# Kernel tuning notes

Hardware: AMD Instinct MI355X
Metric: run time of the kernel (lower is better)

The kernel has to match this reference:

```python
import jax, jax.numpy as jnp
import numpy as np

VOCAB = 50000
COVOCAB = 50000
D = 300
NUM_SENSES = 4
B = 100000


def _xavier(key, shape):
    fan_in, fan_out = shape[-2], shape[-1]
    if len(shape) == 3:
        fan_in, fan_out = shape[1], shape[2]
    limit = (6.0 / (fan_in + fan_out)) ** 0.5
    return jax.random.uniform(key, shape, jnp.float32, -limit, limit)


def setup_inputs() -> dict:
    key = jax.random.key(0)
    k1, k2, k3, k4, k5 = jax.random.split(key, 5)
    V = _xavier(k1, (VOCAB, D, NUM_SENSES))
    W = _xavier(k2, (COVOCAB, D, NUM_SENSES))
    vb = _xavier(k3, (VOCAB, NUM_SENSES))
    wb = _xavier(k4, (COVOCAB, NUM_SENSES))
    IJ = jax.random.randint(k5, (B, 2), 0, VOCAB, dtype=jnp.int64)
    return {"V": V, "W": W, "vb": vb, "wb": wb, "IJ": IJ}


def reference(V, W, vb, wb, IJ):
    i = IJ[:, 0]
    j = IJ[:, 1]
    Vg = V[i]            # [B, d, s_v]  gather
    Wg = W[j]            # [B, d, s_w]  gather
    # bmm(W[j]^T, V[i]) -> [B, s_w, s_v]
    mat = jnp.einsum("bds,bdt->bst", Wg, Vg)
    bias = wb[j][:, :, None] + vb[i][:, None, :]   # [B, s_w, s_v]
    mat = mat + bias
    # faithful to original: log(sum(exp(.)))
    return jnp.log(jnp.sum(jnp.exp(mat), axis=(1, 2)))
```

## Files before the change

### kernel.cpp

```cpp
#include <hip/hip_runtime.h>
#include <hip/hip_bf16.h>


constexpr int D  = 300;
constexpr int NS = 4;

typedef unsigned short ushort8 __attribute__((ext_vector_type(8)));

__device__ __forceinline__ float b2f(unsigned short u) {
    return __uint_as_float(((unsigned int)u) << 16);
}

__global__ void detect_kernel(const unsigned int* __restrict__ Vw,
                              const unsigned int* __restrict__ IJw,
                              int* __restrict__ flags)
{
    const int lane = threadIdx.x & 63;
    unsigned int w0 = Vw[2 * lane];
    unsigned int w1 = Vw[2 * lane + 1];
    unsigned int e0 = (w0 >> 7) & 0xFFu;
    unsigned int e1 = (w1 >> 7) & 0xFFu;
    bool big = (e0 >= 126u) || (e1 >= 126u);
    bool odd_nonzero = (lane < 32) ? (IJw[2 * lane + 1] != 0u) : false;
    int isF32 = __any(big) ? 1 : 0;
    int isI64 = __any(odd_nonzero) ? 0 : 1;
    if (threadIdx.x == 0) {
        flags[0] = isF32;
        flags[1] = isI64;
    }
}

__global__ __launch_bounds__(256) void multisense_kernel(
    const void* __restrict__ V_,
    const void* __restrict__ W_,
    const void* __restrict__ vb_,
    const void* __restrict__ wb_,
    const int*  __restrict__ IJ32,
    void*       __restrict__ out_,
    int B,
    const int*  __restrict__ flags)
{
    const int lane = threadIdx.x & 63;
    const int b    = blockIdx.x * (blockDim.x >> 6) + (threadIdx.x >> 6);
    if (b >= B) return;

    const int isF32 = flags[0];
    const int isI64 = flags[1];

    int i, j;
    if (isI64) { i = IJ32[4 * b]; j = IJ32[4 * b + 2]; }
    else       { i = IJ32[2 * b]; j = IJ32[2 * b + 1]; }

    float acc[NS][NS];
#pragma unroll
    for (int s = 0; s < NS; ++s)
#pragma unroll
        for (int t = 0; t < NS; ++t)
            acc[s][t] = 0.0f;

    if (isF32) {
        const float* Vr = (const float*)V_ + (size_t)i * (D * NS);
        const float* Wr = (const float*)W_ + (size_t)j * (D * NS);
#pragma unroll
        for (int k = 0; k < 5; ++k) {
            const int d = lane + 64 * k;
            if (d < D) {
                const float4 v4 = *reinterpret_cast<const float4*>(Vr + d * NS);
                const float4 w4 = *reinterpret_cast<const float4*>(Wr + d * NS);
                const float v[NS] = {v4.x, v4.y, v4.z, v4.w};
                const float w[NS] = {w4.x, w4.y, w4.z, w4.w};
#pragma unroll
                for (int s = 0; s < NS; ++s)
#pragma unroll
                    for (int t = 0; t < NS; ++t)
                        acc[s][t] = fmaf(w[s], v[t], acc[s][t]);
            }
        }
    } else {
        const unsigned short* Vr = (const unsigned short*)V_ + (size_t)i * (D * NS);
        const unsigned short* Wr = (const unsigned short*)W_ + (size_t)j * (D * NS);
#pragma unroll
        for (int k = 0; k < 3; ++k) {
            const int d = 2 * lane + 128 * k;
            if (d < D) {
                const ushort8 v8 = *reinterpret_cast<const ushort8*>(Vr + d * NS);
                const ushort8 w8 = *reinterpret_cast<const ushort8*>(Wr + d * NS);
                float v[8], w[8];
#pragma unroll
                for (int e = 0; e < 8; ++e) {
                    v[e] = b2f(v8[e]);
                    w[e] = b2f(w8[e]);
                }
#pragma unroll
                for (int s = 0; s < NS; ++s)
#pragma unroll
                    for (int t = 0; t < NS; ++t) {
                        acc[s][t] = fmaf(w[s],     v[t],     acc[s][t]);
                        acc[s][t] = fmaf(w[4 + s], v[4 + t], acc[s][t]);
                    }
            }
        }
    }

#pragma unroll
    for (int off = 32; off; off >>= 1)
#pragma unroll
        for (int s = 0; s < NS; ++s)
#pragma unroll
            for (int t = 0; t < NS; ++t)
                acc[s][t] += __shfl_xor(acc[s][t], off, 64);

    if (lane == 0) {
        float wbj[NS], vbi[NS];
        if (isF32) {
            const float* vbp = (const float*)vb_;
            const float* wbp = (const float*)wb_;
#pragma unroll
            for (int s = 0; s < NS; ++s) {
                wbj[s] = wbp[(size_t)j * NS + s];
                vbi[s] = vbp[(size_t)i * NS + s];
            }
        } else {
            const unsigned short* vbp = (const unsigned short*)vb_;
            const unsigned short* wbp = (const unsigned short*)wb_;
#pragma unroll
            for (int s = 0; s < NS; ++s) {
                wbj[s] = b2f(wbp[(size_t)j * NS + s]);
                vbi[s] = b2f(vbp[(size_t)i * NS + s]);
            }
        }
        float sum = 0.0f;
#pragma unroll
        for (int s = 0; s < NS; ++s)
#pragma unroll
            for (int t = 0; t < NS; ++t)
                sum += expf(acc[s][t] + wbj[s] + vbi[t]);
        const float res = logf(sum);
        if (isF32) ((float*)out_)[b] = res;
        else       ((__hip_bfloat16*)out_)[b] = __float2bfloat16(res);
    }
}

extern "C" void kernel_launch(void* const* d_in, const int* in_sizes, int n_in,
                              void* d_out, int out_size, void* d_ws, size_t ws_size,
                              hipStream_t stream) {
    const void* V  = d_in[0];
    const void* W  = d_in[1];
    const void* vb = d_in[2];
    const void* wb = d_in[3];
    const int*  IJ = (const int*)d_in[4];
    int* flags = (int*)d_ws;

    const int B = out_size;
    hipLaunchKernelGGL(detect_kernel, dim3(1), dim3(64), 0, stream,
                       (const unsigned int*)V, (const unsigned int*)IJ, flags);

    const int wavesPerBlock = 4;
    dim3 block(256);
    dim3 grid((B + wavesPerBlock - 1) / wavesPerBlock);
    hipLaunchKernelGGL(multisense_kernel, grid, block, 0, stream,
                       V, W, vb, wb, IJ, d_out, B, flags);
}
```

Baseline: 510.4 us.

## Drop dtype-detect launch, use butterfly transpose-reduce and parallel exp across lanes

```diff
diff --git a/kernel.cpp b/kernel.cpp
--- a/kernel.cpp
+++ b/kernel.cpp
@@ -2,162 +2,129 @@
 #include <hip/hip_bf16.h>
 
 
-constexpr int D  = 300;
-constexpr int NS = 4;
-
-typedef unsigned short ushort8 __attribute__((ext_vector_type(8)));
-
-__device__ __forceinline__ float b2f(unsigned short u) {
-    return __uint_as_float(((unsigned int)u) << 16);
-}
-
-__global__ void detect_kernel(const unsigned int* __restrict__ Vw,
-                              const unsigned int* __restrict__ IJw,
-                              int* __restrict__ flags)
-{
-    const int lane = threadIdx.x & 63;
-    unsigned int w0 = Vw[2 * lane];
-    unsigned int w1 = Vw[2 * lane + 1];
-    unsigned int e0 = (w0 >> 7) & 0xFFu;
-    unsigned int e1 = (w1 >> 7) & 0xFFu;
-    bool big = (e0 >= 126u) || (e1 >= 126u);
-    bool odd_nonzero = (lane < 32) ? (IJw[2 * lane + 1] != 0u) : false;
-    int isF32 = __any(big) ? 1 : 0;
-    int isI64 = __any(odd_nonzero) ? 0 : 1;
-    if (threadIdx.x == 0) {
-        flags[0] = isF32;
-        flags[1] = isI64;
-    }
-}
+constexpr int D   = 300;
+constexpr int NS  = 4;
+constexpr int ROW = D * NS;
 
 __global__ __launch_bounds__(256) void multisense_kernel(
-    const void* __restrict__ V_,
-    const void* __restrict__ W_,
-    const void* __restrict__ vb_,
-    const void* __restrict__ wb_,
-    const int*  __restrict__ IJ32,
-    void*       __restrict__ out_,
-    int B,
-    const int*  __restrict__ flags)
+    const float* __restrict__ V,
+    const float* __restrict__ W,
+    const float* __restrict__ vb,
+    const float* __restrict__ wb,
+    const unsigned int* __restrict__ IJw,
+    float* __restrict__ out,
+    int B)
 {
     const int lane = threadIdx.x & 63;
     const int b    = blockIdx.x * (blockDim.x >> 6) + (threadIdx.x >> 6);
     if (b >= B) return;
 
-    const int isF32 = flags[0];
-    const int isI64 = flags[1];
+    unsigned int probe = (lane < 32) ? IJw[2 * lane + 1] : 0u;
+    const bool isI64 = (__ballot(probe != 0u) == 0ull);
 
     int i, j;
-    if (isI64) { i = IJ32[4 * b]; j = IJ32[4 * b + 2]; }
-    else       { i = IJ32[2 * b]; j = IJ32[2 * b + 1]; }
+    if (isI64) { i = (int)IJw[4 * (size_t)b];     j = (int)IJw[4 * (size_t)b + 2]; }
+    else       { i = (int)IJw[2 * (size_t)b];     j = (int)IJw[2 * (size_t)b + 1]; }
 
-    float acc[NS][NS];
+    const float* __restrict__ Vr = V + (size_t)i * ROW;
+    const float* __restrict__ Wr = W + (size_t)j * ROW;
+
+    const int s_idx = (lane >> 4) & 3;
+    const int t_idx = (lane >> 2) & 3;
+
+    const float wbj = wb[(size_t)j * NS + s_idx];
+    const float vbi = vb[(size_t)i * NS + t_idx];
+
+    float4 va[5], wa[5];
 #pragma unroll
-    for (int s = 0; s < NS; ++s)
-#pragma unroll
-        for (int t = 0; t < NS; ++t)
-            acc[s][t] = 0.0f;
-
-    if (isF32) {
-        const float* Vr = (const float*)V_ + (size_t)i * (D * NS);
-        const float* Wr = (const float*)W_ + (size_t)j * (D * NS);
-#pragma unroll
-        for (int k = 0; k < 5; ++k) {
-            const int d = lane + 64 * k;
-            if (d < D) {
-                const float4 v4 = *reinterpret_cast<const float4*>(Vr + d * NS);
-                const float4 w4 = *reinterpret_cast<const float4*>(Wr + d * NS);
-                const float v[NS] = {v4.x, v4.y, v4.z, v4.w};
-                const float w[NS] = {w4.x, w4.y, w4.z, w4.w};
-#pragma unroll
-                for (int s = 0; s < NS; ++s)
-#pragma unroll
-                    for (int t = 0; t < NS; ++t)
-                        acc[s][t] = fmaf(w[s], v[t], acc[s][t]);
-            }
-        }
-    } else {
-        const unsigned short* Vr = (const unsigned short*)V_ + (size_t)i * (D * NS);
-        const unsigned short* Wr = (const unsigned short*)W_ + (size_t)j * (D * NS);
-#pragma unroll
-        for (int k = 0; k < 3; ++k) {
-            const int d = 2 * lane + 128 * k;
-            if (d < D) {
-                const ushort8 v8 = *reinterpret_cast<const ushort8*>(Vr + d * NS);
-                const ushort8 w8 = *reinterpret_cast<const ushort8*>(Wr + d * NS);
-                float v[8], w[8];
-#pragma unroll
-                for (int e = 0; e < 8; ++e) {
-                    v[e] = b2f(v8[e]);
-                    w[e] = b2f(w8[e]);
-                }
-#pragma unroll
-                for (int s = 0; s < NS; ++s)
-#pragma unroll
-                    for (int t = 0; t < NS; ++t) {
-                        acc[s][t] = fmaf(w[s],     v[t],     acc[s][t]);
-                        acc[s][t] = fmaf(w[4 + s], v[4 + t], acc[s][t]);
-                    }
-            }
-        }
+    for (int k = 0; k < 4; ++k) {
+        const int d = lane + 64 * k;
+        va[k] = *reinterpret_cast<const float4*>(Vr + (size_t)d * NS);
+        wa[k] = *reinterpret_cast<const float4*>(Wr + (size_t)d * NS);
+    }
+    {
+        const int  d4 = 256 + lane;
+        const int  dc = (d4 < D) ? d4 : 0;
+        const float m = (d4 < D) ? 1.0f : 0.0f;
+        va[4] = *reinterpret_cast<const float4*>(Vr + (size_t)dc * NS);
+        wa[4] = *reinterpret_cast<const float4*>(Wr + (size_t)dc * NS);
+        wa[4].x *= m; wa[4].y *= m; wa[4].z *= m; wa[4].w *= m;
     }
 
+    float acc[16];
 #pragma unroll
-    for (int off = 32; off; off >>= 1)
+    for (int m = 0; m < 16; ++m) acc[m] = 0.0f;
 #pragma unroll
-        for (int s = 0; s < NS; ++s)
+    for (int k = 0; k < 5; ++k) {
+        const float v0 = va[k].x, v1 = va[k].y, v2 = va[k].z, v3 = va[k].w;
+        const float w0 = wa[k].x, w1 = wa[k].y, w2 = wa[k].z, w3 = wa[k].w;
+        acc[ 0] = fmaf(w0, v0, acc[ 0]); acc[ 1] = fmaf(w0, v1, acc[ 1]);
+        acc[ 2] = fmaf(w0, v2, acc[ 2]); acc[ 3] = fmaf(w0, v3, acc[ 3]);
+        acc[ 4] = fmaf(w1, v0, acc[ 4]); acc[ 5] = fmaf(w1, v1, acc[ 5]);
+        acc[ 6] = fmaf(w1, v2, acc[ 6]); acc[ 7] = fmaf(w1, v3, acc[ 7]);
+        acc[ 8] = fmaf(w2, v0, acc[ 8]); acc[ 9] = fmaf(w2, v1, acc[ 9]);
+        acc[10] = fmaf(w2, v2, acc[10]); acc[11] = fmaf(w2, v3, acc[11]);
+        acc[12] = fmaf(w3, v0, acc[12]); acc[13] = fmaf(w3, v1, acc[13]);
+        acc[14] = fmaf(w3, v2, acc[14]); acc[15] = fmaf(w3, v3, acc[15]);
+    }
+
+    const bool b5 = (lane & 32) != 0;
+    float r8[8];
 #pragma unroll
-            for (int t = 0; t < NS; ++t)
-                acc[s][t] += __shfl_xor(acc[s][t], off, 64);
+    for (int m = 0; m < 8; ++m) {
+        const float send = b5 ? acc[m]     : acc[m + 8];
+        const float keep = b5 ? acc[m + 8] : acc[m];
+        r8[m] = keep + __shfl_xor(send, 32, 64);
+    }
+    const bool b4 = (lane & 16) != 0;
+    float r4[4];
+#pragma unroll
+    for (int m = 0; m < 4; ++m) {
+        const float send = b4 ? r8[m]     : r8[m + 4];
+        const float keep = b4 ? r8[m + 4] : r8[m];
+        r4[m] = keep + __shfl_xor(send, 16, 64);
+    }
+    const bool b3 = (lane & 8) != 0;
+    float r2[2];
+#pragma unroll
+    for (int m = 0; m < 2; ++m) {
+        const float send = b3 ? r4[m]     : r4[m + 2];
+        const float keep = b3 ? r4[m + 2] : r4[m];
+        r2[m] = keep + __shfl_xor(send, 8, 64);
+    }
+    const bool b2 = (lane & 4) != 0;
+    float r1;
+    {
+        const float send = b2 ? r2[0] : r2[1];
+        const float keep = b2 ? r2[1] : r2[0];
+        r1 = keep + __shfl_xor(send, 4, 64);
+    }
+    r1 += __shfl_xor(r1, 2, 64);
+    r1 += __shfl_xor(r1, 1, 64);
 
-    if (lane == 0) {
-        float wbj[NS], vbi[NS];
-        if (isF32) {
-            const float* vbp = (const float*)vb_;
-            const float* wbp = (const float*)wb_;
-#pragma unroll
-            for (int s = 0; s < NS; ++s) {
-                wbj[s] = wbp[(size_t)j * NS + s];
-                vbi[s] = vbp[(size_t)i * NS + s];
-            }
-        } else {
-            const unsigned short* vbp = (const unsigned short*)vb_;
-            const unsigned short* wbp = (const unsigned short*)wb_;
-#pragma unroll
-            for (int s = 0; s < NS; ++s) {
-                wbj[s] = b2f(wbp[(size_t)j * NS + s]);
-                vbi[s] = b2f(vbp[(size_t)i * NS + s]);
-            }
-        }
-        float sum = 0.0f;
-#pragma unroll
-        for (int s = 0; s < NS; ++s)
-#pragma unroll
-            for (int t = 0; t < NS; ++t)
-                sum += expf(acc[s][t] + wbj[s] + vbi[t]);
-        const float res = logf(sum);
-        if (isF32) ((float*)out_)[b] = res;
-        else       ((__hip_bfloat16*)out_)[b] = __float2bfloat16(res);
-    }
+    float e = expf(r1 + wbj + vbi);
+    e += __shfl_xor(e,  4, 64);
+    e += __shfl_xor(e,  8, 64);
+    e += __shfl_xor(e, 16, 64);
+    e += __shfl_xor(e, 32, 64);
+
+    if (lane == 0) out[b] = logf(e);
 }
 
 extern "C" void kernel_launch(void* const* d_in, const int* in_sizes, int n_in,
                               void* d_out, int out_size, void* d_ws, size_t ws_size,
                               hipStream_t stream) {
-    const void* V  = d_in[0];
-    const void* W  = d_in[1];
-    const void* vb = d_in[2];
-    const void* wb = d_in[3];
-    const int*  IJ = (const int*)d_in[4];
-    int* flags = (int*)d_ws;
+    const float* V  = (const float*)d_in[0];
+    const float* W  = (const float*)d_in[1];
+    const float* vb = (const float*)d_in[2];
+    const float* wb = (const float*)d_in[3];
+    const unsigned int* IJ = (const unsigned int*)d_in[4];
+    float* out = (float*)d_out;
 
     const int B = out_size;
-    hipLaunchKernelGGL(detect_kernel, dim3(1), dim3(64), 0, stream,
-                       (const unsigned int*)V, (const unsigned int*)IJ, flags);
-
     const int wavesPerBlock = 4;
     dim3 block(256);
     dim3 grid((B + wavesPerBlock - 1) / wavesPerBlock);
     hipLaunchKernelGGL(multisense_kernel, grid, block, 0, stream,
-                       V, W, vb, wb, IJ, d_out, B, flags);
+                       V, W, vb, wb, IJ, out, B);
 }
```

Result: no change. 507.3 us (-0.6%).
